# Kernel optimization log

Hardware: AMD Instinct MI355X
Metric: run time of the kernel (lower is better)

The kernel has to match this reference:

```python
import jax, jax.numpy as jnp
import numpy as np

B, N = 8, 2048
CLIP, D, BD, NC = 512, 256, 128, 10  # CLIP_EMBED_DIM, GNN_NODE_DIM, BOTTLENECK_DIM_GNN, NUM_CLASSES
LN_EPS = 1e-5


def _layer_norm(x, g, b):
    mu = jnp.mean(x, axis=-1, keepdims=True)
    var = jnp.mean(jnp.square(x - mu), axis=-1, keepdims=True)
    return (x - mu) / jnp.sqrt(var + LN_EPS) * g + b


def setup_inputs() -> dict:
    key = jax.random.key(0)
    ks = jax.random.split(key, 16)
    def w(k, shape, fan_in):
        lim = 1.0 / np.sqrt(fan_in)
        return jax.random.uniform(k, shape, jnp.float32, -lim, lim)
    return {
        "local_feat": jax.random.normal(ks[0], (B, N, CLIP), jnp.float32),
        "coords": jax.random.uniform(ks[1], (B, N, 2), jnp.float32),
        "mask": jax.random.randint(ks[2], (B, N), 0, 2).astype(bool),
        # node_encoder: Linear(CLIP->D) + LayerNorm(D)
        "enc_w": w(ks[3], (CLIP, D), CLIP), "enc_b": jnp.zeros((D,), jnp.float32),
        "enc_g": jnp.ones((D,), jnp.float32), "enc_beta": jnp.zeros((D,), jnp.float32),
        "gamma": jnp.asarray(5.0, jnp.float32),  # spatial_gamma
        "wq": w(ks[4], (D, D), D), "bq": jnp.zeros((D,), jnp.float32),
        "wk": w(ks[5], (D, D), D), "bk": jnp.zeros((D,), jnp.float32),
        "wv": w(ks[6], (D, D), D), "bv": jnp.zeros((D,), jnp.float32),
        # bottleneck: Linear(D->BD) + LayerNorm(BD)
        "bn_w": w(ks[7], (D, BD), D), "bn_b": jnp.zeros((BD,), jnp.float32),
        "bn_g": jnp.ones((BD,), jnp.float32), "bn_beta": jnp.zeros((BD,), jnp.float32),
        # classifier: Linear(BD->BD//2) + ReLU + Linear(BD//2->NC)
        "c1_w": w(ks[8], (BD, BD // 2), BD), "c1_b": jnp.zeros((BD // 2,), jnp.float32),
        "c2_w": w(ks[9], (BD // 2, NC), BD // 2), "c2_b": jnp.zeros((NC,), jnp.float32),
    }


def reference(local_feat, coords, mask, enc_w, enc_b, enc_g, enc_beta, gamma,
              wq, bq, wk, bk, wv, bv, bn_w, bn_b, bn_g, bn_beta,
              c1_w, c1_b, c2_w, c2_b):
    # node encoder: Linear + LN + ReLU -> h [B,N,D]
    h = jax.nn.relu(_layer_norm(local_feat @ enc_w + enc_b, enc_g, enc_beta))
    # pairwise euclidean distances on 2D coords (torch.cdist, under no_grad)
    xy = coords[:, :, :2]
    sq = jnp.sum(xy * xy, axis=-1)                                   # [B,N]
    d2 = sq[:, :, None] + sq[:, None, :] - 2.0 * jnp.einsum('bnd,bmd->bnm', xy, xy)
    dist = jax.lax.stop_gradient(jnp.sqrt(jnp.maximum(d2, 0.0)))     # [B,N,N]
    spatial_adj = jnp.exp(-dist * jnp.abs(gamma))
    q, k, v = h @ wq + bq, h @ wk + bk, h @ wv + bv
    scores = jnp.einsum('bnd,bmd->bnm', q, k) / jnp.sqrt(jnp.float32(D))
    attn = jax.nn.softmax(scores, axis=-1) * spatial_adj             # gated attention
    attn = jnp.where(mask[:, None, :], 0.0, attn)                    # zero masked keys
    agg = jnp.einsum('bnm,bmd->bnd', attn, v)                        # [B,N,D]
    out = jax.nn.relu(_layer_norm(agg @ bn_w + bn_b, bn_g, bn_beta)) # [B,N,BD]
    mask_v = (~mask)[:, :, None].astype(out.dtype)                   # [B,N,1]
    pooled = (out * mask_v).sum(axis=1) / jnp.maximum(mask_v.sum(axis=1), 1e-9)
    logits = jax.nn.relu(pooled @ c1_w + c1_b) @ c2_w + c2_b
    return logits, pooled
```

## Files before the change

kernel.cpp:

```cpp
#include <hip/hip_runtime.h>
#include <hip/hip_bf16.h>

typedef unsigned short ushort_t;
typedef __attribute__((ext_vector_type(4))) short s4;
typedef __attribute__((ext_vector_type(8))) short s8;
typedef __attribute__((ext_vector_type(4))) float f4;
typedef __attribute__((ext_vector_type(16))) float f16v;

__device__ __forceinline__ unsigned short f2bf(float f) {
  union { float f; unsigned int u; } c; c.f = f;
  unsigned int r = (c.u + 0x7fffu + ((c.u >> 16) & 1u)) >> 16;
  return (unsigned short)r;
}
__device__ __forceinline__ float bf2f(ushort_t u) {
  union { unsigned int i; float f; } c; c.i = ((unsigned int)u) << 16; return c.f;
}
__device__ __forceinline__ uint4 pack8(float4 a, float4 b) {
  uint4 r;
  r.x = (unsigned)f2bf(a.x) | ((unsigned)f2bf(a.y) << 16);
  r.y = (unsigned)f2bf(a.z) | ((unsigned)f2bf(a.w) << 16);
  r.z = (unsigned)f2bf(b.x) | ((unsigned)f2bf(b.y) << 16);
  r.w = (unsigned)f2bf(b.z) | ((unsigned)f2bf(b.w) << 16);
  return r;
}
__device__ __forceinline__ float fsqrt_fast(float x) {
  float r; asm("v_sqrt_f32 %0, %1" : "=v"(r) : "v"(x)); return r;
}
__device__ __forceinline__ void dma16(const ushort_t* g, const short* l) {
  __builtin_amdgcn_global_load_lds(
      (const __attribute__((address_space(1))) unsigned int*)g,
      (__attribute__((address_space(3))) unsigned int*)(unsigned long)l,
      16, 0, 0);
}

__global__ __launch_bounds__(256) void k_wt_all(
    const float* __restrict__ enc_w, const float* __restrict__ wq,
    const float* __restrict__ wk, const float* __restrict__ wv,
    const float* __restrict__ bn_w,
    ushort_t* __restrict__ enc_wT, ushort_t* __restrict__ wqkvT,
    ushort_t* __restrict__ bn_wT) {
  const int y = blockIdx.y;
  const int i = blockIdx.x * 256 + threadIdx.x;
  if (y == 0) {
    if (i < 131072) { const int n = i >> 9, k = i & 511; enc_wT[i] = f2bf(enc_w[k * 256 + n]); }
  } else if (y <= 3) {
    if (i < 65536) {
      const int n = i >> 8, k = i & 255;
      const float* src = (y == 1) ? wq : (y == 2) ? wk : wv;
      wqkvT[(y - 1) * 65536 + i] = f2bf(src[k * 256 + n]);
    }
  } else {
    if (i < 32768) { const int n = i >> 8, k = i & 255; bn_wT[i] = f2bf(bn_w[k * 128 + n]); }
  }
}

__global__ __launch_bounds__(256, 3) void k_gemm_enc(
    const float* __restrict__ A, const ushort_t* __restrict__ WT,
    const float* __restrict__ bia, const float* __restrict__ g,
    const float* __restrict__ beta, ushort_t* __restrict__ out) {
  __shared__ short Al[32 * 72];
  __shared__ short Bl[256 * 72];
  __shared__ float red1[32][2], red2[32][2];
  const int t = threadIdx.x;
  const int wv = t >> 6, lane = t & 63, l16 = lane & 15, quad = lane >> 4;
  const int wm = wv >> 1, wn = wv & 1;
  const int row0 = blockIdx.x * 32;

  f4 acc[8];
#pragma unroll
  for (int nf = 0; nf < 8; ++nf) acc[nf] = (f4){0.f, 0.f, 0.f, 0.f};

  for (int k0 = 0; k0 < 512; k0 += 64) {
    __syncthreads();
    {
      const int r = t >> 3, c8 = t & 7;
      const float* src = &A[(size_t)(row0 + r) * 512 + k0 + c8 * 8];
      *(uint4*)&Al[r * 72 + c8 * 8] =
          pack8(*(const float4*)src, *(const float4*)(src + 4));
    }
#pragma unroll
    for (int i = 0; i < 8; ++i) {
      const int ch = t + i * 256;
      const int r = ch >> 3, c8 = ch & 7;
      *(uint4*)&Bl[r * 72 + c8 * 8] =
          *(const uint4*)&WT[(size_t)r * 512 + k0 + c8 * 8];
    }
    __syncthreads();
#pragma unroll
    for (int kc = 0; kc < 2; ++kc) {
      const s8 af = *(const s8*)&Al[(wm * 16 + l16) * 72 + kc * 32 + quad * 8];
#pragma unroll
      for (int nf = 0; nf < 8; ++nf) {
        const s8 bf = *(const s8*)&Bl[(wn * 128 + nf * 16 + l16) * 72 + kc * 32 + quad * 8];
        acc[nf] = __builtin_amdgcn_mfma_f32_16x16x32_bf16(af, bf, acc[nf], 0, 0, 0);
      }
    }
  }
  float bi[8], gg[8], bb[8];
#pragma unroll
  for (int nf = 0; nf < 8; ++nf) {
    const int col = wn * 128 + nf * 16 + l16;
    bi[nf] = bia[col]; gg[nf] = g[col]; bb[nf] = beta[col];
  }
  float s1[4] = {0.f, 0.f, 0.f, 0.f}, s2[4] = {0.f, 0.f, 0.f, 0.f};
#pragma unroll
  for (int nf = 0; nf < 8; ++nf)
#pragma unroll
    for (int r = 0; r < 4; ++r) {
      const float v = acc[nf][r] + bi[nf];
      acc[nf][r] = v;
      s1[r] += v; s2[r] += v * v;
    }
#pragma unroll
  for (int m = 1; m < 16; m <<= 1) {
#pragma unroll
    for (int r = 0; r < 4; ++r) {
      s1[r] += __shfl_xor(s1[r], m);
      s2[r] += __shfl_xor(s2[r], m);
    }
  }
  if (l16 == 0) {
#pragma unroll
    for (int r = 0; r < 4; ++r) {
      const int rl = wm * 16 + quad * 4 + r;
      red1[rl][wn] = s1[r]; red2[rl][wn] = s2[r];
    }
  }
  __syncthreads();
#pragma unroll
  for (int r = 0; r < 4; ++r) {
    const int rl = wm * 16 + quad * 4 + r;
    const float mu = (red1[rl][0] + red1[rl][1]) * (1.f / 256.f);
    const float var = (red2[rl][0] + red2[rl][1]) * (1.f / 256.f) - mu * mu;
    const float rstd = rsqrtf(var + 1e-5f);
#pragma unroll
    for (int nf = 0; nf < 8; ++nf) {
      const int col = wn * 128 + nf * 16 + l16;
      const float v = (acc[nf][r] - mu) * rstd * gg[nf] + bb[nf];
      out[(size_t)(row0 + rl) * 256 + col] = f2bf(fmaxf(v, 0.f));
    }
  }
}

__global__ __launch_bounds__(256, 4) void k_gemm_qkv(
    const ushort_t* __restrict__ A, const ushort_t* __restrict__ WT,
    const float* __restrict__ bq, const float* __restrict__ bk,
    const float* __restrict__ bv,
    ushort_t* __restrict__ q, ushort_t* __restrict__ k, ushort_t* __restrict__ vt) {
  __shared__ short Al[64 * 72];
  __shared__ short Bl[128 * 72];
  const int t = threadIdx.x;
  const int wv = t >> 6, lane = t & 63, l16 = lane & 15, quad = lane >> 4;
  const int wm = wv >> 1, wn = wv & 1;
  const int row0 = blockIdx.x * 64;
  const int nb = blockIdx.y;
  const int type = nb >> 1;
  const ushort_t* wtb = WT + (size_t)nb * 128 * 256;

  f4 acc[2][4];
#pragma unroll
  for (int mf = 0; mf < 2; ++mf)
#pragma unroll
    for (int nf = 0; nf < 4; ++nf) acc[mf][nf] = (f4){0.f, 0.f, 0.f, 0.f};

  for (int k0 = 0; k0 < 256; k0 += 64) {
    __syncthreads();
#pragma unroll
    for (int i = 0; i < 2; ++i) {
      const int ch = t + i * 256;
      const int r = ch >> 3, c8 = ch & 7;
      *(uint4*)&Al[r * 72 + c8 * 8] =
          *(const uint4*)&A[(size_t)(row0 + r) * 256 + k0 + c8 * 8];
    }
#pragma unroll
    for (int i = 0; i < 4; ++i) {
      const int ch = t + i * 256;
      const int r = ch >> 3, c8 = ch & 7;
      *(uint4*)&Bl[r * 72 + c8 * 8] =
          *(const uint4*)&wtb[(size_t)r * 256 + k0 + c8 * 8];
    }
    __syncthreads();
#pragma unroll
    for (int kc = 0; kc < 2; ++kc) {
      s8 af[2];
      af[0] = *(const s8*)&Al[(wm * 32 + l16) * 72 + kc * 32 + quad * 8];
      af[1] = *(const s8*)&Al[(wm * 32 + 16 + l16) * 72 + kc * 32 + quad * 8];
#pragma unroll
      for (int nf = 0; nf < 4; ++nf) {
        const s8 bf = *(const s8*)&Bl[(wn * 64 + nf * 16 + l16) * 72 + kc * 32 + quad * 8];
        acc[0][nf] = __builtin_amdgcn_mfma_f32_16x16x32_bf16(af[0], bf, acc[0][nf], 0, 0, 0);
        acc[1][nf] = __builtin_amdgcn_mfma_f32_16x16x32_bf16(af[1], bf, acc[1][nf], 0, 0, 0);
      }
    }
  }
  const float* bias = (type == 0) ? bq : (type == 1) ? bk : bv;
#pragma unroll
  for (int nf = 0; nf < 4; ++nf) {
    const int colg = nb * 128 + wn * 64 + nf * 16 + l16;
    const int col = colg - type * 256;
    const float bi = bias[col];
    if (type == 2) {
      const int b = row0 >> 11;
#pragma unroll
      for (int mf = 0; mf < 2; ++mf) {
        const int n = (row0 & 2047) + wm * 32 + mf * 16 + quad * 4;
        ushort4 pk;
        pk.x = f2bf(acc[mf][nf][0] + bi);
        pk.y = f2bf(acc[mf][nf][1] + bi);
        pk.z = f2bf(acc[mf][nf][2] + bi);
        pk.w = f2bf(acc[mf][nf][3] + bi);
        *(ushort4*)&vt[((size_t)b * 256 + col) * 2048 + n] = pk;
      }
    } else {
      ushort_t* dst = (type == 0) ? q : k;
      const float sc = (type == 0) ? 0.0625f : 1.f;
#pragma unroll
      for (int mf = 0; mf < 2; ++mf)
#pragma unroll
        for (int r = 0; r < 4; ++r) {
          const int row = row0 + wm * 32 + mf * 16 + quad * 4 + r;
          dst[(size_t)row * 256 + col] = f2bf((acc[mf][nf][r] + bi) * sc);
        }
    }
  }
}

__global__ __launch_bounds__(256, 2) void k_attn(
    const ushort_t* __restrict__ qb, const ushort_t* __restrict__ kb,
    const ushort_t* __restrict__ vtb,
    const float* __restrict__ coords, const int* __restrict__ mask,
    const float* __restrict__ gam,
    ushort_t* __restrict__ Opb, float* __restrict__ lws) {
  __shared__ short kld[2][8192];
  __shared__ short vld[2][8192];
  const int t = threadIdx.x;
  const int wv = t >> 6, lane = t & 63, l16 = lane & 15, quad = lane >> 4;
  const int hw = lane >> 5, l32 = lane & 31;
  const int b = blockIdx.z, ks = blockIdx.y;
  const int qw = blockIdx.x * 128 + wv * 32;
  const int kbase = ks * 512;

  float rcx[2], rcy[2];
  {
    const float2 c0 = ((const float2*)coords)[b * 2048 + qw + l16];
    const float2 c1 = ((const float2*)coords)[b * 2048 + qw + 16 + l16];
    rcx[0] = c0.x; rcy[0] = c0.y; rcx[1] = c1.x; rcy[1] = c1.y;
  }
  const float gamma = fabsf(gam[0]);

  f4 o[2][16];
#pragma unroll
  for (int mf = 0; mf < 2; ++mf)
#pragma unroll
    for (int dt = 0; dt < 16; ++dt) o[mf][dt] = (f4){0.f, 0.f, 0.f, 0.f};
  float lrun[2] = {0.f, 0.f};

  const ushort_t* kbb = kb + ((size_t)b * 2048 + kbase) * 256;
  const ushort_t* vbb = vtb + (size_t)b * 256 * 2048 + kbase;
  const ushort_t* qrow0 = qb + ((size_t)b * 2048 + qw + l16) * 256 + quad * 8;
  const ushort_t* qrow1 = qrow0 + 16 * 256;

#pragma unroll
  for (int i = 0; i < 4; ++i) {
    const int i2 = wv * 4 + i;
    dma16(kbb + (size_t)l32 * 256 + (i2 * 2 + hw) * 8, &kld[0][i2 * 512]);
    dma16(vbb + (size_t)(i * 64 + lane) * 2048 + wv * 8, &vld[0][(wv * 256 + i * 64) * 8]);
  }
  __syncthreads();

  for (int kt = 0; kt < 16; ++kt) {
    const int cur = kt & 1;
    const int m0 = kbase + kt * 32;

    s8 qa[2][8];
#pragma unroll
    for (int c = 0; c < 8; ++c) {
      qa[0][c] = *(const s8*)(qrow0 + c * 32);
      qa[1][c] = *(const s8*)(qrow1 + c * 32);
    }
    const float4 kca = *(const float4*)&coords[((size_t)b * 2048 + m0 + quad * 4) * 2];
    const float4 kcb = *(const float4*)&coords[((size_t)b * 2048 + m0 + quad * 4) * 2 + 4];
    const float4 kcc = *(const float4*)&coords[((size_t)b * 2048 + m0 + 16 + quad * 4) * 2];
    const float4 kcd = *(const float4*)&coords[((size_t)b * 2048 + m0 + 16 + quad * 4) * 2 + 4];
    const int4 mq0 = *(const int4*)&mask[b * 2048 + m0 + quad * 4];
    const int4 mq1 = *(const int4*)&mask[b * 2048 + m0 + 16 + quad * 4];

    if (kt < 15) {
      const ushort_t* kn = kbb + (size_t)(kt + 1) * 32 * 256;
      const ushort_t* vn = vbb + (kt + 1) * 32;
      const int nb2 = cur ^ 1;
#pragma unroll
      for (int i = 0; i < 4; ++i) {
        const int i2 = wv * 4 + i;
        dma16(kn + (size_t)l32 * 256 + (i2 * 2 + hw) * 8, &kld[nb2][i2 * 512]);
        dma16(vn + (size_t)(i * 64 + lane) * 2048 + wv * 8, &vld[nb2][(wv * 256 + i * 64) * 8]);
      }
    }

    f4 sc[2][2];
#pragma unroll
    for (int mf = 0; mf < 2; ++mf)
#pragma unroll
      for (int s = 0; s < 2; ++s) sc[mf][s] = (f4){0.f, 0.f, 0.f, 0.f};
#pragma unroll
    for (int c = 0; c < 8; ++c) {
#pragma unroll
      for (int s = 0; s < 2; ++s) {
        const s8 kf = *(const s8*)&kld[cur][((c * 4 + quad) * 32 + s * 16 + l16) * 8];
        sc[0][s] = __builtin_amdgcn_mfma_f32_16x16x32_bf16(kf, qa[0][c], sc[0][s], 0, 0, 0);
        sc[1][s] = __builtin_amdgcn_mfma_f32_16x16x32_bf16(kf, qa[1][c], sc[1][s], 0, 0, 0);
      }
    }

    const float kx[8] = {kca.x, kca.z, kcb.x, kcb.z, kcc.x, kcc.z, kcd.x, kcd.z};
    const float ky[8] = {kca.y, kca.w, kcb.y, kcb.w, kcc.y, kcc.w, kcd.y, kcd.w};
    const int  mk[8] = {mq0.x, mq0.y, mq0.z, mq0.w, mq1.x, mq1.y, mq1.z, mq1.w};
    s8 paf[2];
#pragma unroll
    for (int mf = 0; mf < 2; ++mf) {
      unsigned pu[4];
#pragma unroll
      for (int s = 0; s < 2; ++s) {
#pragma unroll
        for (int rp = 0; rp < 2; ++rp) {
          float wp[2];
#pragma unroll
          for (int e = 0; e < 2; ++e) {
            const int r = rp * 2 + e;
            const int j = s * 4 + r;
            const float p = __expf(sc[mf][s][r]);
            lrun[mf] += p;
            const float dx = rcx[mf] - kx[j], dy = rcy[mf] - ky[j];
            const float dist = fsqrt_fast(dx * dx + dy * dy);
            wp[e] = mk[j] ? 0.f : p * __expf(-gamma * dist);
          }
          pu[s * 2 + rp] = (unsigned)f2bf(wp[0]) | ((unsigned)f2bf(wp[1]) << 16);
        }
      }
      union { s8 v; unsigned u[4]; } cv;
      cv.u[0] = pu[0]; cv.u[1] = pu[1]; cv.u[2] = pu[2]; cv.u[3] = pu[3];
      paf[mf] = cv.v;
    }

#pragma unroll
    for (int dt = 0; dt < 16; ++dt) {
      const int base = ((quad >> 1) * 256 + dt * 16 + l16) * 8 + (quad & 1) * 4;
      const s4 lo = *(const s4*)&vld[cur][base];
      const s4 hi = *(const s4*)&vld[cur][base + 4096];
      const s8 bvf = __builtin_shufflevector(lo, hi, 0, 1, 2, 3, 4, 5, 6, 7);
      o[0][dt] = __builtin_amdgcn_mfma_f32_16x16x32_bf16(paf[0], bvf, o[0][dt], 0, 0, 0);
      o[1][dt] = __builtin_amdgcn_mfma_f32_16x16x32_bf16(paf[1], bvf, o[1][dt], 0, 0, 0);
    }
    __syncthreads();
  }
  ushort_t* OpK = Opb + (size_t)ks * 4194304;
#pragma unroll
  for (int mf = 0; mf < 2; ++mf)
#pragma unroll
    for (int dt = 0; dt < 16; ++dt)
#pragma unroll
      for (int r = 0; r < 4; ++r)
        OpK[((size_t)b * 2048 + qw + mf * 16 + quad * 4 + r) * 256 + dt * 16 + l16] =
            f2bf(o[mf][dt][r]);

#pragma unroll
  for (int mf = 0; mf < 2; ++mf) {
    lrun[mf] += __shfl_xor(lrun[mf], 16);
    lrun[mf] += __shfl_xor(lrun[mf], 32);
  }
  if (quad == 0) {
    lws[ks * 16384 + b * 2048 + qw + l16] = lrun[0];
    lws[ks * 16384 + b * 2048 + qw + 16 + l16] = lrun[1];
  }
}

__global__ __launch_bounds__(256, 3) void k_gemm_bn(
    const ushort_t* __restrict__ Opb, const float* __restrict__ lws,
    const ushort_t* __restrict__ WT,
    const float* __restrict__ bia, const float* __restrict__ g,
    const float* __restrict__ beta, float* __restrict__ pooledAcc) {
  __shared__ short Al[32 * 72];
  __shared__ short Bl[128 * 72];
  __shared__ float red1[32][2], red2[32][2];
  __shared__ float sCm[32];
  const int t = threadIdx.x;
  const int wv = t >> 6, lane = t & 63, l16 = lane & 15, quad = lane >> 4;
  const int wm = wv >> 1, wn = wv & 1;
  const int row0 = blockIdx.x * 32;
  const int b = row0 >> 11;

  if (t < 32) {
    const int row = row0 + t;
    sCm[t] = 1.f / (lws[row] + lws[16384 + row] + lws[32768 + row] + lws[49152 + row]);
  }

  f4 acc[4];
#pragma unroll
  for (int nf = 0; nf < 4; ++nf) acc[nf] = (f4){0.f, 0.f, 0.f, 0.f};

  for (int k0 = 0; k0 < 256; k0 += 64) {
    __syncthreads();
    {
      const int r = t >> 3, c8 = t & 7;
      const float c0 = sCm[r];
      const size_t off = (size_t)(row0 + r) * 256 + k0 + c8 * 8;
      float e[8];
#pragma unroll
      for (int j = 0; j < 8; ++j) e[j] = 0.f;
#pragma unroll
      for (int pp = 0; pp < 4; ++pp) {
        const uint4 u = *(const uint4*)&Opb[(size_t)pp * 4194304 + off];
        e[0] += bf2f((ushort_t)(u.x & 0xffff)); e[1] += bf2f((ushort_t)(u.x >> 16));
        e[2] += bf2f((ushort_t)(u.y & 0xffff)); e[3] += bf2f((ushort_t)(u.y >> 16));
        e[4] += bf2f((ushort_t)(u.z & 0xffff)); e[5] += bf2f((ushort_t)(u.z >> 16));
        e[6] += bf2f((ushort_t)(u.w & 0xffff)); e[7] += bf2f((ushort_t)(u.w >> 16));
      }
      float4 ea = {c0 * e[0], c0 * e[1], c0 * e[2], c0 * e[3]};
      float4 eb = {c0 * e[4], c0 * e[5], c0 * e[6], c0 * e[7]};
      *(uint4*)&Al[r * 72 + c8 * 8] = pack8(ea, eb);
    }
#pragma unroll
    for (int i = 0; i < 4; ++i) {
      const int ch = t + i * 256;
      const int r = ch >> 3, c8 = ch & 7;
      *(uint4*)&Bl[r * 72 + c8 * 8] =
          *(const uint4*)&WT[(size_t)r * 256 + k0 + c8 * 8];
    }
    __syncthreads();
#pragma unroll
    for (int kc = 0; kc < 2; ++kc) {
      const s8 af = *(const s8*)&Al[(wm * 16 + l16) * 72 + kc * 32 + quad * 8];
#pragma unroll
      for (int nf = 0; nf < 4; ++nf) {
        const s8 bf = *(const s8*)&Bl[(wn * 64 + nf * 16 + l16) * 72 + kc * 32 + quad * 8];
        acc[nf] = __builtin_amdgcn_mfma_f32_16x16x32_bf16(af, bf, acc[nf], 0, 0, 0);
      }
    }
  }
  float bi[4], gg[4], bb[4];
#pragma unroll
  for (int nf = 0; nf < 4; ++nf) {
    const int col = wn * 64 + nf * 16 + l16;
    bi[nf] = bia[col]; gg[nf] = g[col]; bb[nf] = beta[col];
  }
  float s1[4] = {0.f, 0.f, 0.f, 0.f}, s2[4] = {0.f, 0.f, 0.f, 0.f};
#pragma unroll
  for (int nf = 0; nf < 4; ++nf)
#pragma unroll
    for (int r = 0; r < 4; ++r) {
      const float v = acc[nf][r] + bi[nf];
      acc[nf][r] = v;
      s1[r] += v; s2[r] += v * v;
    }
#pragma unroll
  for (int m = 1; m < 16; m <<= 1) {
#pragma unroll
    for (int r = 0; r < 4; ++r) {
      s1[r] += __shfl_xor(s1[r], m);
      s2[r] += __shfl_xor(s2[r], m);
    }
  }
  if (l16 == 0) {
#pragma unroll
    for (int r = 0; r < 4; ++r) {
      const int rl = wm * 16 + quad * 4 + r;
      red1[rl][wn] = s1[r]; red2[rl][wn] = s2[r];
    }
  }
  __syncthreads();
#pragma unroll
  for (int r = 0; r < 4; ++r) {
    const int rl = wm * 16 + quad * 4 + r;
    const float mu = (red1[rl][0] + red1[rl][1]) * (1.f / 128.f);
    const float var = (red2[rl][0] + red2[rl][1]) * (1.f / 128.f) - mu * mu;
    const float rstd = rsqrtf(var + 1e-5f);
#pragma unroll
    for (int nf = 0; nf < 4; ++nf) {
      const float v = (acc[nf][r] - mu) * rstd * gg[nf] + bb[nf];
      acc[nf][r] = fmaxf(v, 0.f);
    }
  }
  {
    float mw[4];
#pragma unroll
    for (int r = 0; r < 4; ++r) {
      const int rl = wm * 16 + quad * 4 + r;
      mw[r] = pooledAcc[1024 + row0 + rl];
    }
#pragma unroll
    for (int nf = 0; nf < 4; ++nf) {
      float s = acc[nf][0] * mw[0] + acc[nf][1] * mw[1] +
                acc[nf][2] * mw[2] + acc[nf][3] * mw[3];
      s += __shfl_xor(s, 16);
      s += __shfl_xor(s, 32);
      if (quad == 0) {
        const int col = wn * 64 + nf * 16 + l16;
        atomicAdd(&pooledAcc[b * 128 + col], s);
      }
    }
  }
}

__global__ __launch_bounds__(256) void k_maskf(const int* __restrict__ mask,
                                               float* __restrict__ pooledAcc) {
  const int i = blockIdx.x * 256 + threadIdx.x;
  if (i < 16384) pooledAcc[1024 + i] = mask[i] ? 0.f : 1.f;
  if (i < 1024) pooledAcc[i] = 0.f;
}

__global__ __launch_bounds__(128) void k_pool2_head(
    const float* __restrict__ pooledAcc, const int* __restrict__ mask,
    const float* __restrict__ c1w, const float* __restrict__ c1b,
    const float* __restrict__ c2w, const float* __restrict__ c2b,
    float* __restrict__ dout) {
  __shared__ float ps[128];
  __shared__ float h1[64];
  __shared__ float scnt[128];
  const int b = blockIdx.x, t = threadIdx.x;
  float c = 0.f;
  const int* mb = mask + b * 2048 + t * 16;
#pragma unroll
  for (int j = 0; j < 16; ++j) c += mb[j] ? 0.f : 1.f;
  scnt[t] = c;
  __syncthreads();
  for (int o2 = 64; o2 > 0; o2 >>= 1) {
    if (t < o2) scnt[t] += scnt[t + o2];
    __syncthreads();
  }
  const float cnt = scnt[0];
  const float p = pooledAcc[b * 128 + t] / fmaxf(cnt, 1e-9f);
  ps[t] = p;
  dout[80 + b * 128 + t] = p;
  __syncthreads();
  if (t < 64) {
    float acc = c1b[t];
    for (int d = 0; d < 128; ++d) acc += ps[d] * c1w[d * 64 + t];
    h1[t] = fmaxf(acc, 0.f);
  }
  __syncthreads();
  if (t < 10) {
    float a2 = c2b[t];
    for (int j = 0; j < 64; ++j) a2 += h1[j] * c2w[j * 10 + t];
    dout[b * 10 + t] = a2;
  }
}

extern "C" void kernel_launch(void* const* d_in, const int* in_sizes, int n_in,
                              void* d_out, int out_size, void* d_ws, size_t ws_size,
                              hipStream_t stream) {
  const float* lf     = (const float*)d_in[0];
  const float* coords = (const float*)d_in[1];
  const int*   mask   = (const int*)d_in[2];
  const float* enc_w  = (const float*)d_in[3];
  const float* enc_b  = (const float*)d_in[4];
  const float* enc_g  = (const float*)d_in[5];
  const float* enc_be = (const float*)d_in[6];
  const float* gamma  = (const float*)d_in[7];
  const float* wq     = (const float*)d_in[8];
  const float* bq     = (const float*)d_in[9];
  const float* wk     = (const float*)d_in[10];
  const float* bk     = (const float*)d_in[11];
  const float* wv     = (const float*)d_in[12];
  const float* bv     = (const float*)d_in[13];
  const float* bn_w   = (const float*)d_in[14];
  const float* bn_b   = (const float*)d_in[15];
  const float* bn_g   = (const float*)d_in[16];
  const float* bn_be  = (const float*)d_in[17];
  const float* c1w    = (const float*)d_in[18];
  const float* c1b    = (const float*)d_in[19];
  const float* c2w    = (const float*)d_in[20];
  const float* c2b    = (const float*)d_in[21];

  float* ws = (float*)d_ws;
  ushort_t* h_bf   = (ushort_t*)ws;
  ushort_t* q_bf   = (ushort_t*)(ws + 2097152);
  ushort_t* k_bf   = (ushort_t*)(ws + 4194304);
  ushort_t* vt_bf  = (ushort_t*)(ws + 6291456);
  ushort_t* Opb    = (ushort_t*)(ws + 8388608);
  ushort_t* enc_wT = (ushort_t*)(ws + 17825792);
  ushort_t* wqkvT  = (ushort_t*)(ws + 17891328);
  ushort_t* bn_wT  = (ushort_t*)(ws + 17989632);
  float*    lws    = ws + 18006016;
  float*    pooledAcc = ws + 18071552;
  float* out = (float*)d_out;

  k_wt_all<<<dim3(512, 5), 256, 0, stream>>>(enc_w, wq, wk, wv, bn_w,
                                             enc_wT, wqkvT, bn_wT);
  k_maskf<<<64, 256, 0, stream>>>(mask, pooledAcc);
  k_gemm_enc<<<512, 256, 0, stream>>>(lf, enc_wT, enc_b, enc_g, enc_be, h_bf);
  k_gemm_qkv<<<dim3(256, 6), 256, 0, stream>>>(h_bf, wqkvT, bq, bk, bv, q_bf, k_bf, vt_bf);
  k_attn<<<dim3(16, 4, 8), 256, 0, stream>>>(q_bf, k_bf, vt_bf, coords, mask, gamma,
                                             Opb, lws);
  k_gemm_bn<<<512, 256, 0, stream>>>(Opb, lws, bn_wT, bn_b, bn_g, bn_be, pooledAcc);
  k_pool2_head<<<8, 128, 0, stream>>>(pooledAcc, mask, c1w, c1b, c2w, c2b, out);
}
```

Baseline: 257.6 us.

## Split attention across 8 waves with 16 query rows each and stage key coords/mask in LDS

The attention kernel now runs 512 threads per block, each wave handling 16 query rows instead of 32. This halves per-wave accumulator registers and raises the number of waves sharing each K/V tile in LDS. Query fragments are hoisted out of the key loop, and key coordinates and mask are staged once into shared memory rather than reloaded from global memory each iteration. Exponentials switch to raw exp2 with log2e folded into the Q scaling and gamma. The trade-off is half as much MFMA work per LDS fragment load and more block-wide synchronisation.

```diff
diff --git a/kernel.cpp b/kernel.cpp
--- a/kernel.cpp
+++ b/kernel.cpp
@@ -5,7 +5,6 @@
 typedef __attribute__((ext_vector_type(4))) short s4;
 typedef __attribute__((ext_vector_type(8))) short s8;
 typedef __attribute__((ext_vector_type(4))) float f4;
-typedef __attribute__((ext_vector_type(16))) float f16v;
 
 __device__ __forceinline__ unsigned short f2bf(float f) {
   union { float f; unsigned int u; } c; c.f = f;
@@ -26,12 +25,17 @@
 __device__ __forceinline__ float fsqrt_fast(float x) {
   float r; asm("v_sqrt_f32 %0, %1" : "=v"(r) : "v"(x)); return r;
 }
+__device__ __forceinline__ float fexp2_fast(float x) {
+  float r; asm("v_exp_f32 %0, %1" : "=v"(r) : "v"(x)); return r;
+}
 __device__ __forceinline__ void dma16(const ushort_t* g, const short* l) {
   __builtin_amdgcn_global_load_lds(
       (const __attribute__((address_space(1))) unsigned int*)g,
       (__attribute__((address_space(3))) unsigned int*)(unsigned long)l,
       16, 0, 0);
 }
+
+#define LOG2E 1.44269504f
 
 __global__ __launch_bounds__(256) void k_wt_all(
     const float* __restrict__ enc_w, const float* __restrict__ wq,
@@ -213,7 +217,7 @@
       }
     } else {
       ushort_t* dst = (type == 0) ? q : k;
-      const float sc = (type == 0) ? 0.0625f : 1.f;
+      const float sc = (type == 0) ? (0.0625f * LOG2E) : 1.f;
 #pragma unroll
       for (int mf = 0; mf < 2; ++mf)
 #pragma unroll
@@ -225,7 +229,7 @@
   }
 }
 
-__global__ __launch_bounds__(256, 2) void k_attn(
+__global__ __launch_bounds__(512, 4) void k_attn(
     const ushort_t* __restrict__ qb, const ushort_t* __restrict__ kb,
     const ushort_t* __restrict__ vtb,
     const float* __restrict__ coords, const int* __restrict__ mask,
@@ -233,114 +237,99 @@
     ushort_t* __restrict__ Opb, float* __restrict__ lws) {
   __shared__ short kld[2][8192];
   __shared__ short vld[2][8192];
+  __shared__ __align__(16) float2 cls[512];
+  __shared__ __align__(16) float  mls[512];
   const int t = threadIdx.x;
   const int wv = t >> 6, lane = t & 63, l16 = lane & 15, quad = lane >> 4;
-  const int hw = lane >> 5, l32 = lane & 31;
   const int b = blockIdx.z, ks = blockIdx.y;
-  const int qw = blockIdx.x * 128 + wv * 32;
+  const int qw = blockIdx.x * 128 + wv * 16;
   const int kbase = ks * 512;
-
-  float rcx[2], rcy[2];
-  {
-    const float2 c0 = ((const float2*)coords)[b * 2048 + qw + l16];
-    const float2 c1 = ((const float2*)coords)[b * 2048 + qw + 16 + l16];
-    rcx[0] = c0.x; rcy[0] = c0.y; rcx[1] = c1.x; rcy[1] = c1.y;
-  }
-  const float gamma = fabsf(gam[0]);
-
-  f4 o[2][16];
-#pragma unroll
-  for (int mf = 0; mf < 2; ++mf)
-#pragma unroll
-    for (int dt = 0; dt < 16; ++dt) o[mf][dt] = (f4){0.f, 0.f, 0.f, 0.f};
-  float lrun[2] = {0.f, 0.f};
 
   const ushort_t* kbb = kb + ((size_t)b * 2048 + kbase) * 256;
   const ushort_t* vbb = vtb + (size_t)b * 256 * 2048 + kbase;
-  const ushort_t* qrow0 = qb + ((size_t)b * 2048 + qw + l16) * 256 + quad * 8;
-  const ushort_t* qrow1 = qrow0 + 16 * 256;
-
-#pragma unroll
-  for (int i = 0; i < 4; ++i) {
-    const int i2 = wv * 4 + i;
-    dma16(kbb + (size_t)l32 * 256 + (i2 * 2 + hw) * 8, &kld[0][i2 * 512]);
-    dma16(vbb + (size_t)(i * 64 + lane) * 2048 + wv * 8, &vld[0][(wv * 256 + i * 64) * 8]);
-  }
+
+  {
+    const int key = t & 31, dg = t >> 5;
+    dma16(kbb + (size_t)key * 256 + dg * 8, &kld[0][t * 8]);
+    dma16(kbb + (size_t)key * 256 + dg * 8 + 128, &kld[0][(t + 512) * 8]);
+    const int d = t & 255, kg = t >> 8;
+    dma16(vbb + (size_t)d * 2048 + kg * 8, &vld[0][t * 8]);
+    dma16(vbb + (size_t)d * 2048 + kg * 8 + 16, &vld[0][(t + 512) * 8]);
+  }
+  cls[t] = ((const float2*)coords)[b * 2048 + kbase + t];
+  mls[t] = mask[b * 2048 + kbase + t] ? 0.f : 1.f;
+
+  s8 qa[8];
+  {
+    const ushort_t* qrow = qb + ((size_t)b * 2048 + qw + l16) * 256 + quad * 8;
+#pragma unroll
+    for (int c = 0; c < 8; ++c) qa[c] = *(const s8*)(qrow + c * 32);
+  }
+  float rcx, rcy;
+  {
+    const float2 cc = ((const float2*)coords)[b * 2048 + qw + l16];
+    rcx = cc.x; rcy = cc.y;
+  }
+  const float gl2 = fabsf(gam[0]) * LOG2E;
+
+  f4 o[16];
+#pragma unroll
+  for (int dt = 0; dt < 16; ++dt) o[dt] = (f4){0.f, 0.f, 0.f, 0.f};
+  float lrun = 0.f;
+
   __syncthreads();
 
   for (int kt = 0; kt < 16; ++kt) {
     const int cur = kt & 1;
-    const int m0 = kbase + kt * 32;
-
-    s8 qa[2][8];
-#pragma unroll
-    for (int c = 0; c < 8; ++c) {
-      qa[0][c] = *(const s8*)(qrow0 + c * 32);
-      qa[1][c] = *(const s8*)(qrow1 + c * 32);
-    }
-    const float4 kca = *(const float4*)&coords[((size_t)b * 2048 + m0 + quad * 4) * 2];
-    const float4 kcb = *(const float4*)&coords[((size_t)b * 2048 + m0 + quad * 4) * 2 + 4];
-    const float4 kcc = *(const float4*)&coords[((size_t)b * 2048 + m0 + 16 + quad * 4) * 2];
-    const float4 kcd = *(const float4*)&coords[((size_t)b * 2048 + m0 + 16 + quad * 4) * 2 + 4];
-    const int4 mq0 = *(const int4*)&mask[b * 2048 + m0 + quad * 4];
-    const int4 mq1 = *(const int4*)&mask[b * 2048 + m0 + 16 + quad * 4];
 
     if (kt < 15) {
-      const ushort_t* kn = kbb + (size_t)(kt + 1) * 32 * 256;
+      const ushort_t* kn = kbb + (size_t)(kt + 1) * 8192;
       const ushort_t* vn = vbb + (kt + 1) * 32;
       const int nb2 = cur ^ 1;
-#pragma unroll
-      for (int i = 0; i < 4; ++i) {
-        const int i2 = wv * 4 + i;
-        dma16(kn + (size_t)l32 * 256 + (i2 * 2 + hw) * 8, &kld[nb2][i2 * 512]);
-        dma16(vn + (size_t)(i * 64 + lane) * 2048 + wv * 8, &vld[nb2][(wv * 256 + i * 64) * 8]);
-      }
-    }
-
-    f4 sc[2][2];
-#pragma unroll
-    for (int mf = 0; mf < 2; ++mf)
-#pragma unroll
-      for (int s = 0; s < 2; ++s) sc[mf][s] = (f4){0.f, 0.f, 0.f, 0.f};
+      const int key = t & 31, dg = t >> 5;
+      dma16(kn + (size_t)key * 256 + dg * 8, &kld[nb2][t * 8]);
+      dma16(kn + (size_t)key * 256 + dg * 8 + 128, &kld[nb2][(t + 512) * 8]);
+      const int d = t & 255, kg = t >> 8;
+      dma16(vn + (size_t)d * 2048 + kg * 8, &vld[nb2][t * 8]);
+      dma16(vn + (size_t)d * 2048 + kg * 8 + 16, &vld[nb2][(t + 512) * 8]);
+    }
+
+    f4 sc[2];
+    sc[0] = (f4){0.f, 0.f, 0.f, 0.f};
+    sc[1] = (f4){0.f, 0.f, 0.f, 0.f};
 #pragma unroll
     for (int c = 0; c < 8; ++c) {
-#pragma unroll
-      for (int s = 0; s < 2; ++s) {
-        const s8 kf = *(const s8*)&kld[cur][((c * 4 + quad) * 32 + s * 16 + l16) * 8];
-        sc[0][s] = __builtin_amdgcn_mfma_f32_16x16x32_bf16(kf, qa[0][c], sc[0][s], 0, 0, 0);
-        sc[1][s] = __builtin_amdgcn_mfma_f32_16x16x32_bf16(kf, qa[1][c], sc[1][s], 0, 0, 0);
-      }
-    }
-
-    const float kx[8] = {kca.x, kca.z, kcb.x, kcb.z, kcc.x, kcc.z, kcd.x, kcd.z};
-    const float ky[8] = {kca.y, kca.w, kcb.y, kcb.w, kcc.y, kcc.w, kcd.y, kcd.w};
-    const int  mk[8] = {mq0.x, mq0.y, mq0.z, mq0.w, mq1.x, mq1.y, mq1.z, mq1.w};
-    s8 paf[2];
-#pragma unroll
-    for (int mf = 0; mf < 2; ++mf) {
-      unsigned pu[4];
-#pragma unroll
-      for (int s = 0; s < 2; ++s) {
-#pragma unroll
-        for (int rp = 0; rp < 2; ++rp) {
-          float wp[2];
-#pragma unroll
-          for (int e = 0; e < 2; ++e) {
-            const int r = rp * 2 + e;
-            const int j = s * 4 + r;
-            const float p = __expf(sc[mf][s][r]);
-            lrun[mf] += p;
-            const float dx = rcx[mf] - kx[j], dy = rcy[mf] - ky[j];
-            const float dist = fsqrt_fast(dx * dx + dy * dy);
-            wp[e] = mk[j] ? 0.f : p * __expf(-gamma * dist);
-          }
-          pu[s * 2 + rp] = (unsigned)f2bf(wp[0]) | ((unsigned)f2bf(wp[1]) << 16);
-        }
-      }
-      union { s8 v; unsigned u[4]; } cv;
-      cv.u[0] = pu[0]; cv.u[1] = pu[1]; cv.u[2] = pu[2]; cv.u[3] = pu[3];
-      paf[mf] = cv.v;
-    }
+      const s8 kf0 = *(const s8*)&kld[cur][((c * 4 + quad) * 32 + l16) * 8];
+      sc[0] = __builtin_amdgcn_mfma_f32_16x16x32_bf16(kf0, qa[c], sc[0], 0, 0, 0);
+      const s8 kf1 = *(const s8*)&kld[cur][((c * 4 + quad) * 32 + 16 + l16) * 8];
+      sc[1] = __builtin_amdgcn_mfma_f32_16x16x32_bf16(kf1, qa[c], sc[1], 0, 0, 0);
+    }
+
+    unsigned pu[4];
+#pragma unroll
+    for (int s = 0; s < 2; ++s) {
+      const int k0 = kt * 32 + s * 16 + quad * 4;
+      const float4 c01 = *(const float4*)&cls[k0];
+      const float4 c23 = *(const float4*)&cls[k0 + 2];
+      const float4 mm = *(const float4*)&mls[k0];
+      const float kx[4] = {c01.x, c01.z, c23.x, c23.z};
+      const float ky[4] = {c01.y, c01.w, c23.y, c23.w};
+      const float mv[4] = {mm.x, mm.y, mm.z, mm.w};
+      float w[4];
+#pragma unroll
+      for (int r = 0; r < 4; ++r) {
+        const float p = fexp2_fast(sc[s][r]);
+        lrun += p;
+        const float dx = rcx - kx[r], dy = rcy - ky[r];
+        const float dist = fsqrt_fast(dx * dx + dy * dy);
+        w[r] = p * fexp2_fast(-gl2 * dist) * mv[r];
+      }
+      pu[s * 2 + 0] = (unsigned)f2bf(w[0]) | ((unsigned)f2bf(w[1]) << 16);
+      pu[s * 2 + 1] = (unsigned)f2bf(w[2]) | ((unsigned)f2bf(w[3]) << 16);
+    }
+    union { s8 v; unsigned u[4]; } cv;
+    cv.u[0] = pu[0]; cv.u[1] = pu[1]; cv.u[2] = pu[2]; cv.u[3] = pu[3];
+    const s8 paf = cv.v;
 
 #pragma unroll
     for (int dt = 0; dt < 16; ++dt) {
@@ -348,30 +337,22 @@
       const s4 lo = *(const s4*)&vld[cur][base];
       const s4 hi = *(const s4*)&vld[cur][base + 4096];
       const s8 bvf = __builtin_shufflevector(lo, hi, 0, 1, 2, 3, 4, 5, 6, 7);
-      o[0][dt] = __builtin_amdgcn_mfma_f32_16x16x32_bf16(paf[0], bvf, o[0][dt], 0, 0, 0);
-      o[1][dt] = __builtin_amdgcn_mfma_f32_16x16x32_bf16(paf[1], bvf, o[1][dt], 0, 0, 0);
-    }
-    __syncthreads();
-  }
+      o[dt] = __builtin_amdgcn_mfma_f32_16x16x32_bf16(paf, bvf, o[dt], 0, 0, 0);
+    }
+    __syncthreads();
+  }
+
   ushort_t* OpK = Opb + (size_t)ks * 4194304;
 #pragma unroll
-  for (int mf = 0; mf < 2; ++mf)
-#pragma unroll
-    for (int dt = 0; dt < 16; ++dt)
-#pragma unroll
-      for (int r = 0; r < 4; ++r)
-        OpK[((size_t)b * 2048 + qw + mf * 16 + quad * 4 + r) * 256 + dt * 16 + l16] =
-            f2bf(o[mf][dt][r]);
-
-#pragma unroll
-  for (int mf = 0; mf < 2; ++mf) {
-    lrun[mf] += __shfl_xor(lrun[mf], 16);
-    lrun[mf] += __shfl_xor(lrun[mf], 32);
-  }
-  if (quad == 0) {
-    lws[ks * 16384 + b * 2048 + qw + l16] = lrun[0];
-    lws[ks * 16384 + b * 2048 + qw + 16 + l16] = lrun[1];
-  }
+  for (int dt = 0; dt < 16; ++dt)
+#pragma unroll
+    for (int r = 0; r < 4; ++r)
+      OpK[((size_t)b * 2048 + qw + quad * 4 + r) * 256 + dt * 16 + l16] =
+          f2bf(o[dt][r]);
+
+  lrun += __shfl_xor(lrun, 16);
+  lrun += __shfl_xor(lrun, 32);
+  if (quad == 0) lws[ks * 16384 + b * 2048 + qw + l16] = lrun;
 }
 
 __global__ __launch_bounds__(256, 3) void k_gemm_bn(
@@ -589,7 +570,7 @@
   k_maskf<<<64, 256, 0, stream>>>(mask, pooledAcc);
   k_gemm_enc<<<512, 256, 0, stream>>>(lf, enc_wT, enc_b, enc_g, enc_be, h_bf);
   k_gemm_qkv<<<dim3(256, 6), 256, 0, stream>>>(h_bf, wqkvT, bq, bk, bv, q_bf, k_bf, vt_bf);
-  k_attn<<<dim3(16, 4, 8), 256, 0, stream>>>(q_bf, k_bf, vt_bf, coords, mask, gamma,
+  k_attn<<<dim3(16, 4, 8), 512, 0, stream>>>(q_bf, k_bf, vt_bf, coords, mask, gamma,
                                              Opb, lws);
   k_gemm_bn<<<512, 256, 0, stream>>>(Opb, lws, bn_wT, bn_b, bn_g, bn_be, pooledAcc);
   k_pool2_head<<<8, 128, 0, stream>>>(pooledAcc, mask, c1w, c1b, c2w, c2b, out);
```

New measurement: 235.9 us. 1.09x faster.
